# Performance work log

Measured on AMD Instinct MI355X. Metric: run time of the kernel, lower is better.

## Reference

```python
import jax, jax.numpy as jnp
import numpy as np

B, T, D_IN, HID, NB, NCLS = 256, 512, 64, 64, 10, 2


def ferro_basis(x, centers, widths, coeffs):
    """KAN-style ferroelectric basis expansion.
    x: (N, in_dim); centers/widths: (num_basis,); coeffs: (in_dim, num_basis, out_dim)
    returns (N, out_dim).
    """
    phi = jnp.tanh((x[..., None] - centers) / widths)  # (N, in_dim, num_basis)
    return jnp.einsum('bik,iko->bo', phi, coeffs)


def setup_inputs() -> dict:
    key = jax.random.key(0)
    ks = jax.random.split(key, 8)
    sc = 1.0 / np.sqrt(D_IN * NB)
    inp = {
        'x': jax.random.normal(ks[0], (B, T, D_IN), dtype=jnp.float32),
        'lift_centers': jnp.linspace(-1.0, 1.0, NB, dtype=jnp.float32),
        'lift_widths': jnp.full((NB,), 0.5, dtype=jnp.float32),
        'lift_coeffs': jax.random.normal(ks[1], (D_IN, NB, HID), dtype=jnp.float32) * sc,
        'rnn_centers': jnp.linspace(-1.0, 1.0, NB, dtype=jnp.float32),
        'rnn_widths': jnp.full((NB,), 0.5, dtype=jnp.float32),
        'rnn_coeffs': jax.random.normal(ks[2], (HID, NB, HID), dtype=jnp.float32) * (1.0 / np.sqrt(HID * NB)),
        'head_centers': jnp.linspace(-1.0, 1.0, NB, dtype=jnp.float32),
        'head_widths': jnp.full((NB,), 0.5, dtype=jnp.float32),
        'head_coeffs': jax.random.normal(ks[3], (HID, NB, HID), dtype=jnp.float32) * (1.0 / np.sqrt(HID * NB)),
        'head_W': jax.random.normal(ks[4], (HID, NCLS), dtype=jnp.float32) * (1.0 / np.sqrt(HID)),
        'head_b': jnp.zeros((NCLS,), dtype=jnp.float32),
    }
    return inp


def reference(x, lift_centers, lift_widths, lift_coeffs,
              rnn_centers, rnn_widths, rnn_coeffs,
              head_centers, head_widths, head_coeffs,
              head_W, head_b):
    b, t, d = x.shape
    # NODE_Encoder: t = linspace(0, T, steps=1) -> single time point, so odeint
    # returns h0 unchanged; z_t == lift(x_t). Lift applied to every timestep
    # (as in the original per-t loop), vectorized over B*T.
    z = ferro_basis(x.reshape(b * t, d), lift_centers, lift_widths, lift_coeffs)
    z = z.reshape(b, t, -1)  # (B, T, HID)
    # FullyNonlinearKANCell: combined[:, :hidden] == x_phi, so h_t = sigmoid(input_basis(z_t));
    # the recurrence is degenerate and the final h depends only on the last timestep.
    h = jax.nn.sigmoid(ferro_basis(z[:, -1, :], rnn_centers, rnn_widths, rnn_coeffs))
    # dropout: eval mode -> identity
    phi = jax.nn.sigmoid(ferro_basis(h, head_centers, head_widths, head_coeffs))
    logits = phi @ head_W + head_b  # (B, num_classes)
    return logits
```

## Files before the change

kernel.cpp:

```cpp
#include <hip/hip_runtime.h>
#include <math.h>

#define BB    256
#define TT    512
#define DIN   64
#define HIDD  64
#define NBAS  10
#define NCLS  2

#define NTHR   1024
#define NWAVES (NTHR / 64)
#define NPHI   (DIN * NBAS)
#define EPT    (NPHI / NWAVES)

__global__ __launch_bounds__(NTHR) void kan_fwd(
    const float* __restrict__ x,
    const float* __restrict__ lift_c, const float* __restrict__ lift_w, const float* __restrict__ lift_coef,
    const float* __restrict__ rnn_c,  const float* __restrict__ rnn_w,  const float* __restrict__ rnn_coef,
    const float* __restrict__ head_c, const float* __restrict__ head_w, const float* __restrict__ head_coef,
    const float* __restrict__ W, const float* __restrict__ bvec,
    float* __restrict__ out)
{
    const int b = blockIdx.x;
    const int t = threadIdx.x;
    const int o = t & 63;
    const int w = t >> 6;

    __shared__ float act[DIN];
    __shared__ float phi[NPHI];
    __shared__ float part[NWAVES][DIN];

    if (t < DIN)
        act[t] = x[((size_t)b * TT + (TT - 1)) * DIN + t];

    auto layer = [&](const float* __restrict__ cptr,
                     const float* __restrict__ wptr,
                     const float* __restrict__ coef,
                     bool sig) {
        __syncthreads();
        if (t < NPHI) {
            const int i = t / NBAS;
            const int k = t - i * NBAS;
            phi[t] = tanhf((act[i] - cptr[k]) / wptr[k]);
        }
        __syncthreads();

        float a0 = 0.0f, a1 = 0.0f;
        const int e0 = w * EPT;
        const float* cp = coef + (size_t)e0 * HIDD + o;
        #pragma unroll
        for (int e = 0; e < EPT; e += 2) {
            a0 = fmaf(phi[e0 + e],     cp[(e)     * HIDD], a0);
            a1 = fmaf(phi[e0 + e + 1], cp[(e + 1) * HIDD], a1);
        }
        part[w][o] = a0 + a1;
        __syncthreads();

        if (t < DIN) {
            float s = 0.0f;
            #pragma unroll
            for (int ww = 0; ww < NWAVES; ++ww) s += part[ww][t];
            if (sig) s = 1.0f / (1.0f + expf(-s));
            act[t] = s;
        }
    };

    layer(lift_c, lift_w, lift_coef, false);
    layer(rnn_c,  rnn_w,  rnn_coef,  true);
    layer(head_c, head_w, head_coef, true);

    if (t < DIN) {
        const float cur = act[t];
        float p0 = cur * W[t * NCLS + 0];
        float p1 = cur * W[t * NCLS + 1];
        #pragma unroll
        for (int off = 32; off > 0; off >>= 1) {
            p0 += __shfl_down(p0, off);
            p1 += __shfl_down(p1, off);
        }
        if (t == 0) {
            out[b * NCLS + 0] = p0 + bvec[0];
            out[b * NCLS + 1] = p1 + bvec[1];
        }
    }
}

extern "C" void kernel_launch(void* const* d_in, const int* in_sizes, int n_in,
                              void* d_out, int out_size, void* d_ws, size_t ws_size,
                              hipStream_t stream) {
    const float* x          = (const float*)d_in[0];
    const float* lift_c     = (const float*)d_in[1];
    const float* lift_w     = (const float*)d_in[2];
    const float* lift_coef  = (const float*)d_in[3];
    const float* rnn_c      = (const float*)d_in[4];
    const float* rnn_w      = (const float*)d_in[5];
    const float* rnn_coef   = (const float*)d_in[6];
    const float* head_c     = (const float*)d_in[7];
    const float* head_w     = (const float*)d_in[8];
    const float* head_coef  = (const float*)d_in[9];
    const float* W          = (const float*)d_in[10];
    const float* bvec       = (const float*)d_in[11];
    float* out              = (float*)d_out;

    kan_fwd<<<dim3(BB), dim3(NTHR), 0, stream>>>(
        x, lift_c, lift_w, lift_coef,
        rnn_c, rnn_w, rnn_coef,
        head_c, head_w, head_coef,
        W, bvec, out);
}
```

Before: 12.64 us.

## Prefetch coefficients into registers and compute basis per wave via shuffles

Coefficients for all three layers are loaded into registers early, so the global loads overlap with the x load and earlier layers instead of sitting serially inside each layer. The shared phi buffer and its barrier are removed. Each wave computes only its own 40 tanh basis values and broadcasts them with lane shuffles, and the divides become multiplies by precomputed reciprocals. This trades higher register pressure (three 40-element arrays, launch bound hint) for fewer syncs and less exposed memory latency.

```diff
diff --git a/kernel.cpp b/kernel.cpp
--- a/kernel.cpp
+++ b/kernel.cpp
@@ -9,11 +9,11 @@
 #define NCLS  2
 
 #define NTHR   1024
-#define NWAVES (NTHR / 64)
+#define NWAVES 16
 #define NPHI   (DIN * NBAS)
 #define EPT    (NPHI / NWAVES)
 
-__global__ __launch_bounds__(NTHR) void kan_fwd(
+__global__ __launch_bounds__(NTHR, 4) void kan_fwd(
     const float* __restrict__ x,
     const float* __restrict__ lift_c, const float* __restrict__ lift_w, const float* __restrict__ lift_coef,
     const float* __restrict__ rnn_c,  const float* __restrict__ rnn_w,  const float* __restrict__ rnn_coef,
@@ -27,52 +27,82 @@
     const int w = t >> 6;
 
     __shared__ float act[DIN];
-    __shared__ float phi[NPHI];
     __shared__ float part[NWAVES][DIN];
 
-    if (t < DIN)
-        act[t] = x[((size_t)b * TT + (TT - 1)) * DIN + t];
+    float xv = 0.0f;
+    if (t < DIN) xv = x[((size_t)b * TT + (TT - 1)) * DIN + t];
 
-    auto layer = [&](const float* __restrict__ cptr,
-                     const float* __restrict__ wptr,
-                     const float* __restrict__ coef,
-                     bool sig) {
-        __syncthreads();
-        if (t < NPHI) {
-            const int i = t / NBAS;
-            const int k = t - i * NBAS;
-            phi[t] = tanhf((act[i] - cptr[k]) / wptr[k]);
-        }
-        __syncthreads();
+    const int li = o / NBAS;
+    const int lk = o - li * NBAS;
+    const float lc = lift_c[lk], liw = 1.0f / lift_w[lk];
+    const float rc = rnn_c[lk],  riw = 1.0f / rnn_w[lk];
+    const float hc = head_c[lk], hiw = 1.0f / head_w[lk];
+    float W0 = 0.0f, W1 = 0.0f;
+    if (t < DIN) { W0 = W[t * NCLS + 0]; W1 = W[t * NCLS + 1]; }
 
+    const int e0 = w * EPT;
+    const float* cpA = lift_coef + (size_t)e0 * HIDD + o;
+    const float* cpB = rnn_coef  + (size_t)e0 * HIDD + o;
+    const float* cpC = head_coef + (size_t)e0 * HIDD + o;
+
+    float cA[EPT], cB[EPT];
+    #pragma unroll
+    for (int e = 0; e < EPT; ++e) cA[e] = cpA[e * HIDD];
+    #pragma unroll
+    for (int e = 0; e < EPT; ++e) cB[e] = cpB[e * HIDD];
+
+    if (t < DIN) act[t] = xv;
+    __syncthreads();
+
+    auto contract = [&](float pv, const float (&cr)[EPT]) -> float {
         float a0 = 0.0f, a1 = 0.0f;
-        const int e0 = w * EPT;
-        const float* cp = coef + (size_t)e0 * HIDD + o;
         #pragma unroll
         for (int e = 0; e < EPT; e += 2) {
-            a0 = fmaf(phi[e0 + e],     cp[(e)     * HIDD], a0);
-            a1 = fmaf(phi[e0 + e + 1], cp[(e + 1) * HIDD], a1);
+            a0 = fmaf(__shfl(pv, e),     cr[e],     a0);
+            a1 = fmaf(__shfl(pv, e + 1), cr[e + 1], a1);
         }
-        part[w][o] = a0 + a1;
-        __syncthreads();
-
-        if (t < DIN) {
-            float s = 0.0f;
-            #pragma unroll
-            for (int ww = 0; ww < NWAVES; ++ww) s += part[ww][t];
-            if (sig) s = 1.0f / (1.0f + expf(-s));
-            act[t] = s;
-        }
+        return a0 + a1;
     };
 
-    layer(lift_c, lift_w, lift_coef, false);
-    layer(rnn_c,  rnn_w,  rnn_coef,  true);
-    layer(head_c, head_w, head_coef, true);
+    float pv = 0.0f;
+    if (o < EPT) pv = tanhf((act[(w << 2) + li] - lc) * liw);
+    float cC[EPT];
+    #pragma unroll
+    for (int e = 0; e < EPT; ++e) cC[e] = cpC[e * HIDD];
 
+    part[w][o] = contract(pv, cA);
+    __syncthreads();
     if (t < DIN) {
-        const float cur = act[t];
-        float p0 = cur * W[t * NCLS + 0];
-        float p1 = cur * W[t * NCLS + 1];
+        float s = 0.0f;
+        #pragma unroll
+        for (int ww = 0; ww < NWAVES; ++ww) s += part[ww][t];
+        act[t] = s;
+    }
+    __syncthreads();
+
+    pv = 0.0f;
+    if (o < EPT) pv = tanhf((act[(w << 2) + li] - rc) * riw);
+    part[w][o] = contract(pv, cB);
+    __syncthreads();
+    if (t < DIN) {
+        float s = 0.0f;
+        #pragma unroll
+        for (int ww = 0; ww < NWAVES; ++ww) s += part[ww][t];
+        act[t] = 1.0f / (1.0f + expf(-s));
+    }
+    __syncthreads();
+
+    pv = 0.0f;
+    if (o < EPT) pv = tanhf((act[(w << 2) + li] - hc) * hiw);
+    part[w][o] = contract(pv, cC);
+    __syncthreads();
+    if (t < DIN) {
+        float s = 0.0f;
+        #pragma unroll
+        for (int ww = 0; ww < NWAVES; ++ww) s += part[ww][t];
+        s = 1.0f / (1.0f + expf(-s));
+        float p0 = s * W0;
+        float p1 = s * W1;
         #pragma unroll
         for (int off = 32; off > 0; off >>= 1) {
             p0 += __shfl_down(p0, off);
```

Measured after the change: 23.38 us. +84.9%, slower.

## Batch four samples per block with float4 coefficient loads and shuffle reductions

Applied to the files above, without the earlier changes.

Each block now processes four batch rows instead of one, so every coefficient loaded from global memory is reused across four samples. The grid shrinks to 64 blocks. The matvec uses float4 coefficient loads with a transposed phi layout in shared memory, and partial sums are combined with cross-lane xor shuffles before the shared-memory reduction. Fewer blocks than CUs may leave the GPU underoccupied, and each thread now does more serial work per layer.

```diff
diff --git a/kernel.cpp b/kernel.cpp
--- a/kernel.cpp
+++ b/kernel.cpp
@@ -8,10 +8,13 @@
 #define NBAS  10
 #define NCLS  2
 
+#define G      4
+#define NBLK   (BB / G)
 #define NTHR   1024
-#define NWAVES (NTHR / 64)
+#define NWAVES 16
 #define NPHI   (DIN * NBAS)
 #define EPT    (NPHI / NWAVES)
+#define NF4    (EPT / 4)
 
 __global__ __launch_bounds__(NTHR) void kan_fwd(
     const float* __restrict__ x,
@@ -21,66 +24,109 @@
     const float* __restrict__ W, const float* __restrict__ bvec,
     float* __restrict__ out)
 {
-    const int b = blockIdx.x;
-    const int t = threadIdx.x;
-    const int o = t & 63;
-    const int w = t >> 6;
+    const int b    = blockIdx.x;
+    const int t    = threadIdx.x;
+    const int l    = t & 63;
+    const int w    = t >> 6;
+    const int esub = l >> 4;
+    const int og   = (l & 15) << 2;
 
-    __shared__ float act[DIN];
-    __shared__ float phi[NPHI];
-    __shared__ float part[NWAVES][DIN];
+    __shared__ __align__(16) float act[G][DIN];
+    __shared__ __align__(16) float phiT[NPHI][G];
+    __shared__ __align__(16) float part[NWAVES][G][DIN];
 
-    if (t < DIN)
-        act[t] = x[((size_t)b * TT + (TT - 1)) * DIN + t];
+    if (t < G * DIN) {
+        const int g = t >> 6, i = t & 63;
+        act[g][i] = x[((size_t)(G * b + g) * TT + (TT - 1)) * DIN + i];
+    }
 
-    auto layer = [&](const float* __restrict__ cptr,
-                     const float* __restrict__ wptr,
-                     const float* __restrict__ coef,
-                     bool sig) {
-        __syncthreads();
-        if (t < NPHI) {
-            const int i = t / NBAS;
-            const int k = t - i * NBAS;
-            phi[t] = tanhf((act[i] - cptr[k]) / wptr[k]);
+    const int idx0 = t, idx1 = t + NTHR, idx2 = t + 2 * NTHR;
+    const int g0 = idx0 / NPHI, r0 = idx0 - g0 * NPHI, i0 = r0 / NBAS, k0 = r0 - i0 * NBAS;
+    const int g1 = idx1 / NPHI, r1 = idx1 - g1 * NPHI, i1 = r1 / NBAS, k1 = r1 - i1 * NBAS;
+    const int g2 = idx2 / NPHI, r2 = idx2 - g2 * NPHI, i2 = r2 / NBAS, k2 = r2 - i2 * NBAS;
+    const bool has2 = (t < (G * NPHI - 2 * NTHR));
+
+    const int e0 = w * EPT + esub;
+    const float4* fA = (const float4*)lift_coef + (size_t)e0 * 16 + (og >> 2);
+    const float4* fB = (const float4*)rnn_coef  + (size_t)e0 * 16 + (og >> 2);
+    const float4* fC = (const float4*)head_coef + (size_t)e0 * 16 + (og >> 2);
+
+    __syncthreads();
+
+    auto layer = [&](const float* __restrict__ cptr, const float* __restrict__ wptr,
+                     const float4* __restrict__ f4, bool sig, bool store_act) -> float {
+        {
+            const float c0v = cptr[k0], w0v = 1.0f / wptr[k0];
+            const float c1v = cptr[k1], w1v = 1.0f / wptr[k1];
+            phiT[r0][g0] = tanhf((act[g0][i0] - c0v) * w0v);
+            phiT[r1][g1] = tanhf((act[g1][i1] - c1v) * w1v);
+            if (has2) {
+                const float c2v = cptr[k2], w2v = 1.0f / wptr[k2];
+                phiT[r2][g2] = tanhf((act[g2][i2] - c2v) * w2v);
+            }
         }
         __syncthreads();
 
-        float a0 = 0.0f, a1 = 0.0f;
-        const int e0 = w * EPT;
-        const float* cp = coef + (size_t)e0 * HIDD + o;
+        float4 acc[G];
         #pragma unroll
-        for (int e = 0; e < EPT; e += 2) {
-            a0 = fmaf(phi[e0 + e],     cp[(e)     * HIDD], a0);
-            a1 = fmaf(phi[e0 + e + 1], cp[(e + 1) * HIDD], a1);
+        for (int g = 0; g < G; ++g) acc[g] = make_float4(0.f, 0.f, 0.f, 0.f);
+        #pragma unroll
+        for (int j = 0; j < NF4; ++j) {
+            const float4 cf = f4[j * 64];
+            const float4 ph = *(const float4*)&phiT[e0 + 4 * j][0];
+            acc[0].x = fmaf(ph.x, cf.x, acc[0].x); acc[0].y = fmaf(ph.x, cf.y, acc[0].y);
+            acc[0].z = fmaf(ph.x, cf.z, acc[0].z); acc[0].w = fmaf(ph.x, cf.w, acc[0].w);
+            acc[1].x = fmaf(ph.y, cf.x, acc[1].x); acc[1].y = fmaf(ph.y, cf.y, acc[1].y);
+            acc[1].z = fmaf(ph.y, cf.z, acc[1].z); acc[1].w = fmaf(ph.y, cf.w, acc[1].w);
+            acc[2].x = fmaf(ph.z, cf.x, acc[2].x); acc[2].y = fmaf(ph.z, cf.y, acc[2].y);
+            acc[2].z = fmaf(ph.z, cf.z, acc[2].z); acc[2].w = fmaf(ph.z, cf.w, acc[2].w);
+            acc[3].x = fmaf(ph.w, cf.x, acc[3].x); acc[3].y = fmaf(ph.w, cf.y, acc[3].y);
+            acc[3].z = fmaf(ph.w, cf.z, acc[3].z); acc[3].w = fmaf(ph.w, cf.w, acc[3].w);
         }
-        part[w][o] = a0 + a1;
+        #pragma unroll
+        for (int off = 16; off < 64; off <<= 1) {
+            #pragma unroll
+            for (int g = 0; g < G; ++g) {
+                acc[g].x += __shfl_xor(acc[g].x, off);
+                acc[g].y += __shfl_xor(acc[g].y, off);
+                acc[g].z += __shfl_xor(acc[g].z, off);
+                acc[g].w += __shfl_xor(acc[g].w, off);
+            }
+        }
+        if (esub == 0) {
+            #pragma unroll
+            for (int g = 0; g < G; ++g) *(float4*)&part[w][g][og] = acc[g];
+        }
         __syncthreads();
 
-        if (t < DIN) {
-            float s = 0.0f;
+        float s = 0.0f;
+        if (t < G * DIN) {
+            const int g = t >> 6, o = t & 63;
             #pragma unroll
-            for (int ww = 0; ww < NWAVES; ++ww) s += part[ww][t];
+            for (int ww = 0; ww < NWAVES; ++ww) s += part[ww][g][o];
             if (sig) s = 1.0f / (1.0f + expf(-s));
-            act[t] = s;
+            if (store_act) act[g][o] = s;
         }
+        __syncthreads();
+        return s;
     };
 
-    layer(lift_c, lift_w, lift_coef, false);
-    layer(rnn_c,  rnn_w,  rnn_coef,  true);
-    layer(head_c, head_w, head_coef, true);
+    layer(lift_c, lift_w, fA, false, true);
+    layer(rnn_c,  rnn_w,  fB, true,  true);
+    const float s3 = layer(head_c, head_w, fC, true, false);
 
-    if (t < DIN) {
-        const float cur = act[t];
-        float p0 = cur * W[t * NCLS + 0];
-        float p1 = cur * W[t * NCLS + 1];
+    if (t < G * DIN) {
+        const int g = t >> 6, o = t & 63;
+        float p0 = s3 * W[o * NCLS + 0];
+        float p1 = s3 * W[o * NCLS + 1];
         #pragma unroll
         for (int off = 32; off > 0; off >>= 1) {
             p0 += __shfl_down(p0, off);
             p1 += __shfl_down(p1, off);
         }
-        if (t == 0) {
-            out[b * NCLS + 0] = p0 + bvec[0];
-            out[b * NCLS + 1] = p1 + bvec[1];
+        if (o == 0) {
+            out[(G * b + g) * NCLS + 0] = p0 + bvec[0];
+            out[(G * b + g) * NCLS + 1] = p1 + bvec[1];
         }
     }
 }
@@ -102,7 +148,7 @@
     const float* bvec       = (const float*)d_in[11];
     float* out              = (float*)d_out;
 
-    kan_fwd<<<dim3(BB), dim3(NTHR), 0, stream>>>(
+    kan_fwd<<<dim3(NBLK), dim3(NTHR), 0, stream>>>(
         x, lift_c, lift_w, lift_coef,
         rnn_c, rnn_w, rnn_coef,
         head_c, head_w, head_coef,
```

Measured after the change: 17.23 us. +36.3%, slower.

## Shrink block to 4 waves, prefetch next layer's coeffs as float4 registers, shuffle phi

Applied to the files above, without the earlier changes.

Cuts the block from 1024 to 256 threads. Each lane computes its own tanh basis values and broadcasts them with wave shuffles instead of staging them in shared memory, and coefficient rows are loaded as float4 into registers. The next layer's coefficients are prefetched before the current layer's reduction and barrier, so load latency overlaps the serial layer chain. Center and width parameters and the head weights are loaded up front, and division is replaced by a reciprocal multiply. The risk is heavy register use (120 float4 registers across the three prefetch buffers) and fewer waves to hide latency.

```diff
diff --git a/kernel.cpp b/kernel.cpp
--- a/kernel.cpp
+++ b/kernel.cpp
@@ -8,12 +8,16 @@
 #define NBAS  10
 #define NCLS  2
 
-#define NTHR   1024
-#define NWAVES (NTHR / 64)
-#define NPHI   (DIN * NBAS)
-#define EPT    (NPHI / NWAVES)
+#define NTHR  256
+#define NW    4
+#define EPW   160
+#define NF4   40
 
-__global__ __launch_bounds__(NTHR) void kan_fwd(
+__device__ __forceinline__ float sigmoidf_(float v) {
+    return 1.0f / (1.0f + expf(-v));
+}
+
+__global__ __launch_bounds__(NTHR, 1) void kan_fwd(
     const float* __restrict__ x,
     const float* __restrict__ lift_c, const float* __restrict__ lift_w, const float* __restrict__ lift_coef,
     const float* __restrict__ rnn_c,  const float* __restrict__ rnn_w,  const float* __restrict__ rnn_coef,
@@ -21,58 +25,124 @@
     const float* __restrict__ W, const float* __restrict__ bvec,
     float* __restrict__ out)
 {
-    const int b = blockIdx.x;
-    const int t = threadIdx.x;
-    const int o = t & 63;
-    const int w = t >> 6;
+    const int b    = blockIdx.x;
+    const int t    = threadIdx.x;
+    const int l    = t & 63;
+    const int w    = t >> 6;
+    const int esub = l >> 4;
+    const int og   = (l & 15) << 2;
 
     __shared__ float act[DIN];
-    __shared__ float phi[NPHI];
-    __shared__ float part[NWAVES][DIN];
+    __shared__ __align__(16) float part[NW][DIN];
 
+    const int i0 = (w << 4) + l / NBAS,          k0 = l % NBAS;
+    const int i1 = (w << 4) + (64 + l) / NBAS,   k1 = (64 + l) % NBAS;
+    const int i2 = (w << 4) + (128 + l) / NBAS,  k2 = (128 + l) % NBAS;
+
+    const float* xb = x + ((size_t)b * TT + (TT - 1)) * DIN;
+    const float x0 = xb[i0];
+    const float x1 = xb[i1];
+    const float x2 = (l < 32) ? xb[i2] : 0.0f;
+
+    const float lc0 = lift_c[k0], lw0 = 1.0f / lift_w[k0];
+    const float lc1 = lift_c[k1], lw1 = 1.0f / lift_w[k1];
+    const float lc2 = lift_c[k2], lw2 = 1.0f / lift_w[k2];
+    const float rc0 = rnn_c[k0],  rw0 = 1.0f / rnn_w[k0];
+    const float rc1 = rnn_c[k1],  rw1 = 1.0f / rnn_w[k1];
+    const float rc2 = rnn_c[k2],  rw2 = 1.0f / rnn_w[k2];
+    const float hc0 = head_c[k0], hw0 = 1.0f / head_w[k0];
+    const float hc1 = head_c[k1], hw1 = 1.0f / head_w[k1];
+    const float hc2 = head_c[k2], hw2 = 1.0f / head_w[k2];
+    float W0 = 0.0f, W1 = 0.0f;
+    if (t < DIN) { W0 = W[t * NCLS + 0]; W1 = W[t * NCLS + 1]; }
+
+    const size_t fbase = (size_t)(EPW * w + esub) * 16 + (og >> 2);
+    const float4* fA = (const float4*)lift_coef + fbase;
+    const float4* fB = (const float4*)rnn_coef  + fbase;
+    const float4* fC = (const float4*)head_coef + fbase;
+
+    #define CONTRACT(ACC, PV0, PV1, PV2, CARR)                                  \
+        {                                                                       \
+            _Pragma("unroll")                                                   \
+            for (int j = 0; j < NF4; ++j) {                                     \
+                float pj;                                                       \
+                if (j < 16)      pj = __shfl((PV0), esub + 4 * j);              \
+                else if (j < 32) pj = __shfl((PV1), esub + 4 * j - 64);         \
+                else             pj = __shfl((PV2), esub + 4 * j - 128);        \
+                const float4 cf = (CARR)[j];                                    \
+                (ACC).x = fmaf(pj, cf.x, (ACC).x);                              \
+                (ACC).y = fmaf(pj, cf.y, (ACC).y);                              \
+                (ACC).z = fmaf(pj, cf.z, (ACC).z);                              \
+                (ACC).w = fmaf(pj, cf.w, (ACC).w);                              \
+            }                                                                   \
+        }
+
+    #define XREDUCE(ACC)                                                        \
+        {                                                                       \
+            _Pragma("unroll")                                                   \
+            for (int off = 16; off < 64; off <<= 1) {                           \
+                (ACC).x += __shfl_xor((ACC).x, off);                            \
+                (ACC).y += __shfl_xor((ACC).y, off);                            \
+                (ACC).z += __shfl_xor((ACC).z, off);                            \
+                (ACC).w += __shfl_xor((ACC).w, off);                            \
+            }                                                                   \
+        }
+
+    float4 c1[NF4];
+    #pragma unroll
+    for (int j = 0; j < NF4; ++j) c1[j] = fA[j * 64];
+
+    float pv0 = tanhf((x0 - lc0) * lw0);
+    float pv1 = tanhf((x1 - lc1) * lw1);
+    float pv2 = (l < 32) ? tanhf((x2 - lc2) * lw2) : 0.0f;
+
+    float4 a = make_float4(0.f, 0.f, 0.f, 0.f);
+    CONTRACT(a, pv0, pv1, pv2, c1);
+
+    float4 c2[NF4];
+    #pragma unroll
+    for (int j = 0; j < NF4; ++j) c2[j] = fB[j * 64];
+
+    XREDUCE(a);
+    if (esub == 0) *(float4*)&part[w][og] = a;
+    __syncthreads();
     if (t < DIN)
-        act[t] = x[((size_t)b * TT + (TT - 1)) * DIN + t];
+        act[t] = part[0][t] + part[1][t] + part[2][t] + part[3][t];
+    __syncthreads();
 
-    auto layer = [&](const float* __restrict__ cptr,
-                     const float* __restrict__ wptr,
-                     const float* __restrict__ coef,
-                     bool sig) {
-        __syncthreads();
-        if (t < NPHI) {
-            const int i = t / NBAS;
-            const int k = t - i * NBAS;
-            phi[t] = tanhf((act[i] - cptr[k]) / wptr[k]);
-        }
-        __syncthreads();
+    pv0 = tanhf((act[i0] - rc0) * rw0);
+    pv1 = tanhf((act[i1] - rc1) * rw1);
+    pv2 = (l < 32) ? tanhf((act[i2] - rc2) * rw2) : 0.0f;
 
-        float a0 = 0.0f, a1 = 0.0f;
-        const int e0 = w * EPT;
-        const float* cp = coef + (size_t)e0 * HIDD + o;
-        #pragma unroll
-        for (int e = 0; e < EPT; e += 2) {
-            a0 = fmaf(phi[e0 + e],     cp[(e)     * HIDD], a0);
-            a1 = fmaf(phi[e0 + e + 1], cp[(e + 1) * HIDD], a1);
-        }
-        part[w][o] = a0 + a1;
-        __syncthreads();
+    a = make_float4(0.f, 0.f, 0.f, 0.f);
+    CONTRACT(a, pv0, pv1, pv2, c2);
 
-        if (t < DIN) {
-            float s = 0.0f;
-            #pragma unroll
-            for (int ww = 0; ww < NWAVES; ++ww) s += part[ww][t];
-            if (sig) s = 1.0f / (1.0f + expf(-s));
-            act[t] = s;
-        }
-    };
+    float4 c3[NF4];
+    #pragma unroll
+    for (int j = 0; j < NF4; ++j) c3[j] = fC[j * 64];
 
-    layer(lift_c, lift_w, lift_coef, false);
-    layer(rnn_c,  rnn_w,  rnn_coef,  true);
-    layer(head_c, head_w, head_coef, true);
+    XREDUCE(a);
+    if (esub == 0) *(float4*)&part[w][og] = a;
+    __syncthreads();
+    if (t < DIN)
+        act[t] = sigmoidf_(part[0][t] + part[1][t] + part[2][t] + part[3][t]);
+    __syncthreads();
+
+    pv0 = tanhf((act[i0] - hc0) * hw0);
+    pv1 = tanhf((act[i1] - hc1) * hw1);
+    pv2 = (l < 32) ? tanhf((act[i2] - hc2) * hw2) : 0.0f;
+
+    a = make_float4(0.f, 0.f, 0.f, 0.f);
+    CONTRACT(a, pv0, pv1, pv2, c3);
+    XREDUCE(a);
+    if (esub == 0) *(float4*)&part[w][og] = a;
+    __syncthreads();
 
     if (t < DIN) {
-        const float cur = act[t];
-        float p0 = cur * W[t * NCLS + 0];
-        float p1 = cur * W[t * NCLS + 1];
+        float s = part[0][t] + part[1][t] + part[2][t] + part[3][t];
+        s = sigmoidf_(s);
+        float p0 = s * W0;
+        float p1 = s * W1;
         #pragma unroll
         for (int off = 32; off > 0; off >>= 1) {
             p0 += __shfl_down(p0, off);
@@ -83,6 +153,9 @@
             out[b * NCLS + 1] = p1 + bvec[1];
         }
     }
+
+    #undef CONTRACT
+    #undef XREDUCE
 }
 
 extern "C" void kernel_launch(void* const* d_in, const int* in_sizes, int n_in,
```

Measured after the change: 13.69 us. 1.08x slower.
